# Kernel optimization log

Hardware: AMD Instinct MI355X
Metric: run time of the kernel (lower is better)

The kernel has to match this reference:

```python
import jax, jax.numpy as jnp
import numpy as np

B, S_IMG, S_TXT, D, H, HD = 1, 2048, 512, 3072, 24, 128
EMB, N_IP = 4096, 64
IP_SCALE = 1.0
EPS = 1e-6
SM_SCALE = 1.0 / np.sqrt(HD).astype(np.float32)


def _lin(x, W, b=None):
    # torch Linear: y = x @ W.T + b, W: [out, in]
    y = jnp.einsum('bsd,od->bso', x, W)
    return y if b is None else y + b


def _heads(x):  # [B,S,D] -> [B,H,S,HD]
    return x.reshape(B, -1, H, HD).transpose(0, 2, 1, 3)


def _rms(x, w):
    return x * jax.lax.rsqrt(jnp.mean(x * x, axis=-1, keepdims=True) + EPS) * w


def _rope(x, cos, sin):
    # interleaved real/imag rotation, cos/sin: [S, HD] broadcast over B,H
    xr = x.reshape(*x.shape[:-1], HD // 2, 2)
    rot = jnp.stack([-xr[..., 1], xr[..., 0]], axis=-1).reshape(x.shape)
    return x * cos + rot * sin


def _sdpa(q, k, v):
    s = jnp.einsum('bhqd,bhkd->bhqk', q, k) * SM_SCALE
    p = jax.nn.softmax(s, axis=-1)
    return jnp.einsum('bhqk,bhkd->bhqd', p, v)


def setup_inputs() -> dict:
    key = jax.random.key(0)
    ks = jax.random.split(key, 32)
    r = lambda i, shape: jax.random.normal(ks[i], shape, dtype=jnp.float32)
    w = lambda i, shape: r(i, shape) * 0.02
    inp = {
        'hidden_states': r(0, (B, S_IMG, D)),
        'encoder_hidden_states': r(1, (B, S_TXT, D)),
        'image_embeds': r(2, (B, N_IP, EMB)),
        'rope_cos': jnp.cos(r(3, (S_TXT + S_IMG, HD))),
        'rope_sin': jnp.sin(r(3, (S_TXT + S_IMG, HD))),
        'Wq': w(4, (D, D)), 'bq': jnp.zeros((D,)),
        'Wk': w(5, (D, D)), 'bk': jnp.zeros((D,)),
        'Wv': w(6, (D, D)), 'bv': jnp.zeros((D,)),
        'Waq': w(7, (D, D)), 'baq': jnp.zeros((D,)),
        'Wak': w(8, (D, D)), 'bak': jnp.zeros((D,)),
        'Wav': w(9, (D, D)), 'bav': jnp.zeros((D,)),
        'Wo': w(10, (D, D)), 'bo': jnp.zeros((D,)),
        'Wao': w(11, (D, D)), 'bao': jnp.zeros((D,)),
        'norm_q_w': jnp.ones((HD,)), 'norm_k_w': jnp.ones((HD,)),
        'norm_aq_w': jnp.ones((HD,)), 'norm_ak_w': jnp.ones((HD,)),
        'Wk_ip': w(12, (D, EMB)), 'Wv_ip': w(13, (D, EMB)),
        'txt_seq_len': S_TXT,
    }
    return inp


def reference(hidden_states, encoder_hidden_states, image_embeds, rope_cos, rope_sin,
              Wq, bq, Wk, bk, Wv, bv, Waq, baq, Wak, bak, Wav, bav,
              Wo, bo, Wao, bao, norm_q_w, norm_k_w, norm_aq_w, norm_ak_w,
              Wk_ip, Wv_ip, txt_seq_len):
    # main stream projections + per-head RMSNorm
    q = _rms(_heads(_lin(hidden_states, Wq, bq)), norm_q_w)
    k = _rms(_heads(_lin(hidden_states, Wk, bk)), norm_k_w)
    v = _heads(_lin(hidden_states, Wv, bv))
    # encoder (text) stream projections + RMSNorm, concat text before image
    eq = _rms(_heads(_lin(encoder_hidden_states, Waq, baq)), norm_aq_w)
    ek = _rms(_heads(_lin(encoder_hidden_states, Wak, bak)), norm_ak_w)
    ev = _heads(_lin(encoder_hidden_states, Wav, bav))
    q = jnp.concatenate([eq, q], axis=2)
    k = jnp.concatenate([ek, k], axis=2)
    v = jnp.concatenate([ev, v], axis=2)
    # IP-adapter branch uses pre-RoPE image-token queries
    ip_q = q[:, :, txt_seq_len:]
    ip_k = _heads(_lin(image_embeds, Wk_ip))
    ip_v = _heads(_lin(image_embeds, Wv_ip))
    ip_hs = _sdpa(ip_q, ip_k, ip_v).transpose(0, 2, 1, 3).reshape(B, -1, H * HD)
    # rotary on joint q/k, then main attention
    q = _rope(q, rope_cos, rope_sin)
    k = _rope(k, rope_cos, rope_sin)
    hs = _sdpa(q, k, v).transpose(0, 2, 1, 3).reshape(B, -1, H * HD)
    # add scaled IP-adapter output to the image part
    img = hs[:, txt_seq_len:] + IP_SCALE * ip_hs
    enc = hs[:, :txt_seq_len]
    # output projections
    out_img = _lin(img, Wo, bo)
    out_enc = _lin(enc, Wao, bao)
    return out_img, out_enc
```

## Files before the change

### kernel.cpp

```cpp
#include <hip/hip_runtime.h>
#include <hip/hip_bf16.h>

#define H 24
#define HD 128
#define DMODEL 3072
#define S_IMG 2048
#define S_TXT 512
#define S_ALL 2560
#define EMB 4096
#define N_IP 64
#define SM_SCALE 0.08838834764831845f

typedef __attribute__((ext_vector_type(8))) short short8;
typedef __attribute__((ext_vector_type(4))) float f32x4;
typedef __attribute__((ext_vector_type(16))) float f32x16;

__device__ inline unsigned short f2bf(float f) {
    unsigned u = __builtin_bit_cast(unsigned, f);
    return (unsigned short)((u + 0x7fffu + ((u >> 16) & 1u)) >> 16);
}
__device__ inline unsigned pk2(float a, float b) {
    return (unsigned)f2bf(a) | ((unsigned)f2bf(b) << 16);
}
__device__ inline float bf2f(unsigned short u) {
    unsigned x = ((unsigned)u) << 16;
    return __builtin_bit_cast(float, x);
}

__device__ inline void gload16(const void* g, void* l) {
    __builtin_amdgcn_global_load_lds(
        (const __attribute__((address_space(1))) unsigned int*)g,
        (__attribute__((address_space(3))) unsigned int*)(unsigned int)(unsigned long long)l,
        16, 0, 0);
}

struct CastSegs {
    const float* src[13];
    unsigned short* dst[13];
    int n8[13];
    int ntot8[13];
    int bstart[14];
};

__global__ __launch_bounds__(256)
void castall(CastSegs cs)
{
    int b = blockIdx.x, seg = 0;
    while (seg < 12 && b >= cs.bstart[seg + 1]) seg++;
    int nb = cs.bstart[seg + 1] - cs.bstart[seg];
    int lb = b - cs.bstart[seg];
    const float* in = cs.src[seg];
    unsigned short* out = cs.dst[seg];
    int n8 = cs.n8[seg], ntot = cs.ntot8[seg];
    for (int i = lb * 256 + threadIdx.x; i < ntot; i += nb * 256) {
        int4 o;
        if (i < n8) {
            const float4* p = (const float4*)(in + (size_t)i * 8);
            float4 a = p[0], bb = p[1];
            o.x = pk2(a.x, a.y); o.y = pk2(a.z, a.w);
            o.z = pk2(bb.x, bb.y); o.w = pk2(bb.z, bb.w);
        } else {
            o.x = 0; o.y = 0; o.z = 0; o.w = 0;
        }
        *(int4*)(out + (size_t)i * 8) = o;
    }
}

__global__ __launch_bounds__(256)
void bcat2(const float* __restrict__ q0, const float* __restrict__ k0, const float* __restrict__ v0,
           const float* __restrict__ q1, const float* __restrict__ k1, const float* __restrict__ v1,
           float* __restrict__ d0, float* __restrict__ d1)
{
    int i = blockIdx.x * 256 + threadIdx.x;
    int which = i >= 3 * DMODEL;
    int j = which ? i - 3 * DMODEL : i;
    const float* a = which ? q1 : q0;
    const float* b = which ? k1 : k0;
    const float* c = which ? v1 : v0;
    float v = (j < DMODEL) ? a[j] : ((j < 2 * DMODEL) ? b[j - DMODEL] : c[j - 2 * DMODEL]);
    (which ? d1 : d0)[j] = v;
}

template<int OUTBF>
__global__ __launch_bounds__(256)
void gemmx(const unsigned short* __restrict__ A0, const unsigned short* __restrict__ B0,
           const float* __restrict__ b0, void* __restrict__ C0,
           const unsigned short* __restrict__ A1, const unsigned short* __restrict__ B1,
           const float* __restrict__ b1, void* __restrict__ C1,
           int mbSplit, int N, int K, int nbm, int GN)
{
    __shared__ unsigned short sm[2 * 8192];
    const int tid = threadIdx.x, lane = tid & 63, wid = tid >> 6;
    const int wr = wid >> 1, wc = wid & 1;
    const int r15 = lane & 15, g = lane >> 4;

    int nwg = gridDim.x;
    int t = (blockIdx.x & 7) * (nwg >> 3) + (blockIdx.x >> 3);
    int gsz = nbm * GN;
    int G = t / gsz, l = t - G * gsz;
    int mb = l % nbm, nb = G * GN + l / nbm;

    const unsigned short* A; const unsigned short* B; const float* bias; void* C; int mrow;
    if (mb < mbSplit) { A = A0; B = B0; bias = b0; C = C0; mrow = mb; }
    else             { A = A1; B = B1; bias = b1; C = C1; mrow = mb - mbSplit; }
    const int m0 = mrow * 128, n0 = nb * 128;

    const int lr = lane >> 3;
    const int lc = lane & 7;
    const int gcol = ((lc * 16) ^ (lr << 4)) >> 1;

    const unsigned short* Ab = A + (size_t)(m0 + wid * 32 + lr) * K + gcol;
    const unsigned short* Bb = B + (size_t)(n0 + wid * 32 + lr) * K + gcol;
    char* smc = (char*)sm;

    f32x4 acc[4][4];
    #pragma unroll
    for (int i = 0; i < 4; i++)
        #pragma unroll
        for (int j = 0; j < 4; j++)
            acc[i][j] = {0.f, 0.f, 0.f, 0.f};

    for (int k0 = 0; k0 < K; k0 += 64) {
        #pragma unroll
        for (int cc = 0; cc < 4; cc++) {
            gload16(Ab + (size_t)cc * 8 * K + k0, smc + (wid * 32 + cc * 8) * 128);
            gload16(Bb + (size_t)cc * 8 * K + k0, smc + 16384 + (wid * 32 + cc * 8) * 128);
        }
        __syncthreads();
        #pragma unroll
        for (int ks = 0; ks < 2; ks++) {
            short8 af[4], bf[4];
            #pragma unroll
            for (int mi = 0; mi < 4; mi++) {
                int row = wr * 64 + mi * 16 + r15;
                af[mi] = *(const short8*)(smc + row * 128 + ((ks * 64 + g * 16) ^ ((row & 7) << 4)));
            }
            #pragma unroll
            for (int ni = 0; ni < 4; ni++) {
                int row = wc * 64 + ni * 16 + r15;
                bf[ni] = *(const short8*)(smc + 16384 + row * 128 + ((ks * 64 + g * 16) ^ ((row & 7) << 4)));
            }
            #pragma unroll
            for (int mi = 0; mi < 4; mi++)
                #pragma unroll
                for (int ni = 0; ni < 4; ni++)
                    acc[mi][ni] = __builtin_amdgcn_mfma_f32_16x16x32_bf16(af[mi], bf[ni], acc[mi][ni], 0, 0, 0);
        }
        __syncthreads();
    }
    #pragma unroll
    for (int mi = 0; mi < 4; mi++) {
        #pragma unroll
        for (int ni = 0; ni < 4; ni++) {
            int col = n0 + wc * 64 + ni * 16 + r15;
            float bv = bias ? bias[col] : 0.f;
            #pragma unroll
            for (int r = 0; r < 4; r++) {
                int grow = m0 + wr * 64 + mi * 16 + g * 4 + r;
                float v = acc[mi][ni][r] + bv;
                if (OUTBF)
                    ((unsigned short*)C)[(size_t)grow * N + col] = f2bf(v);
                else
                    ((float*)C)[(size_t)grow * N + col] = v;
            }
        }
    }
}

__global__ __launch_bounds__(256)
void rmsropeQK(const unsigned short* __restrict__ qkvb,
               const float* __restrict__ nqw, const float* __restrict__ nkw,
               const float* __restrict__ naqw, const float* __restrict__ nakw,
               const float* __restrict__ cosb, const float* __restrict__ sinb,
               unsigned short* __restrict__ qb, unsigned short* __restrict__ kb,
               unsigned short* __restrict__ ipq)
{
    int wg = blockIdx.x * 4 + (threadIdx.x >> 6);
    int lane = threadIdx.x & 63;
    int s = wg / H, h = wg - s * H;
    const unsigned short* row = qkvb + (size_t)s * (3 * DMODEL);
    unsigned uq = *(const unsigned*)(row + h * HD + lane * 2);
    unsigned uk = *(const unsigned*)(row + DMODEL + h * HD + lane * 2);
    float q0 = bf2f((unsigned short)uq), q1 = bf2f((unsigned short)(uq >> 16));
    float k0 = bf2f((unsigned short)uk), k1 = bf2f((unsigned short)(uk >> 16));
    float sq = q0 * q0 + q1 * q1, sk = k0 * k0 + k1 * k1;
    #pragma unroll
    for (int off = 1; off < 64; off <<= 1) {
        sq += __shfl_xor(sq, off);
        sk += __shfl_xor(sk, off);
    }
    float rq = rsqrtf(sq * (1.f / HD) + 1e-6f) * SM_SCALE;
    float rk = rsqrtf(sk * (1.f / HD) + 1e-6f);
    const float* wq = (s < S_TXT) ? naqw : nqw;
    const float* wk = (s < S_TXT) ? nakw : nkw;
    float xq0 = q0 * rq * wq[lane * 2], xq1 = q1 * rq * wq[lane * 2 + 1];
    float xk0 = k0 * rk * wk[lane * 2], xk1 = k1 * rk * wk[lane * 2 + 1];
    if (s >= S_TXT)
        *(unsigned*)(ipq + (size_t)h * S_IMG * HD + (size_t)(s - S_TXT) * HD + lane * 2) = pk2(xq0, xq1);
    float c0 = cosb[s * HD + lane * 2], c1 = cosb[s * HD + lane * 2 + 1];
    float s0 = sinb[s * HD + lane * 2], s1 = sinb[s * HD + lane * 2 + 1];
    *(unsigned*)(qb + (size_t)h * S_ALL * HD + (size_t)s * HD + lane * 2) =
        pk2(xq0 * c0 - xq1 * s0, xq1 * c1 + xq0 * s1);
    *(unsigned*)(kb + (size_t)h * S_ALL * HD + (size_t)s * HD + lane * 2) =
        pk2(xk0 * c0 - xk1 * s0, xk1 * c1 + xk0 * s1);
}

__global__ __launch_bounds__(256)
void vtrans(const unsigned short* __restrict__ src, int stride,
            unsigned short* __restrict__ vt, int Stot)
{
    __shared__ unsigned short lv[64 * 130];
    int h = blockIdx.y;
    int s0 = blockIdx.x * 64;
    const unsigned short* base = src + (size_t)s0 * stride + h * HD;
    int tid = threadIdx.x;
    #pragma unroll
    for (int i = 0; i < 4; i++) {
        int slot = tid + 256 * i;
        int row = slot >> 4, c = slot & 15;
        int4 v = *(const int4*)(base + (size_t)row * stride + c * 8);
        unsigned* p = (unsigned*)(lv + row * 130 + c * 8);
        p[0] = (unsigned)v.x; p[1] = (unsigned)v.y; p[2] = (unsigned)v.z; p[3] = (unsigned)v.w;
    }
    __syncthreads();
    #pragma unroll
    for (int i = 0; i < 4; i++) {
        int slot = tid + 256 * i;
        int d = slot >> 3, c8 = slot & 7;
        unsigned w0 = lv[(c8 * 8 + 0) * 130 + d] | ((unsigned)lv[(c8 * 8 + 1) * 130 + d] << 16);
        unsigned w1 = lv[(c8 * 8 + 2) * 130 + d] | ((unsigned)lv[(c8 * 8 + 3) * 130 + d] << 16);
        unsigned w2 = lv[(c8 * 8 + 4) * 130 + d] | ((unsigned)lv[(c8 * 8 + 5) * 130 + d] << 16);
        unsigned w3 = lv[(c8 * 8 + 6) * 130 + d] | ((unsigned)lv[(c8 * 8 + 7) * 130 + d] << 16);
        int4 o = {(int)w0, (int)w1, (int)w2, (int)w3};
        *(int4*)(vt + (size_t)(h * HD + d) * Stot + s0 + c8 * 8) = o;
    }
}

__global__ __launch_bounds__(256)
void cast_heads8(const unsigned short* __restrict__ in, unsigned short* __restrict__ out)
{
    int idx = blockIdx.x * 256 + threadIdx.x;
    int s = idx / 384;
    int rem = idx - s * 384;
    int h = rem >> 4, d8 = rem & 15;
    int4 v = *(const int4*)(in + (size_t)s * (2 * DMODEL) + h * HD + d8 * 8);
    *(int4*)(out + ((size_t)h * N_IP + s) * HD + d8 * 8) = v;
}

template<int MODE>
__global__ __launch_bounds__(512, 2)
void flash2(const unsigned short* __restrict__ Q, const unsigned short* __restrict__ Kb,
            const unsigned short* __restrict__ Vt, const unsigned short* __restrict__ ipb,
            unsigned short* __restrict__ Out, int Sq, int Skv)
{
    __shared__ char sm[33792];
    const int h = blockIdx.y;
    const int q0 = blockIdx.x * 256;
    const int tid = threadIdx.x, w = tid >> 6, lane = tid & 63;
    const int l31 = lane & 31, hi = lane >> 5;

    const unsigned short* Qh = Q + ((size_t)h * Sq + q0 + w * 32 + l31) * HD + hi * 8;
    short8 qf[8];
    #pragma unroll
    for (int c = 0; c < 8; c++)
        qf[c] = *(const short8*)(Qh + c * 16);

    float m = -3.0e38f, lsum = 0.f;
    f32x16 o[4];
    #pragma unroll
    for (int dn = 0; dn < 4; dn++)
        #pragma unroll
        for (int r = 0; r < 16; r++) o[dn][r] = 0.f;

    const unsigned short* Kh = Kb + (size_t)h * Skv * HD;
    const unsigned short* Vth = Vt + (size_t)h * HD * Skv;
    float* scl = (float*)(sm + 32768) + w * 32;

    for (int kv0 = 0; kv0 < Skv; kv0 += 64) {
        #pragma unroll
        for (int cc = 0; cc < 2; cc++) {
            int flat = w * 128 + cc * 64 + lane;
            int row = flat >> 4, slot = flat & 15;
            gload16(Kh + (size_t)(kv0 + row) * HD + (((slot * 16) ^ ((row & 7) << 4)) >> 1),
                    sm + w * 2048 + cc * 1024);
        }
        #pragma unroll
        for (int cc = 0; cc < 2; cc++) {
            int flat = w * 128 + cc * 64 + lane;
            int d = flat >> 3, slot = flat & 7;
            gload16(Vth + (size_t)d * Skv + kv0 + (((slot * 16) ^ ((d & 7) << 4)) >> 1),
                    sm + 16384 + w * 2048 + cc * 1024);
        }
        __syncthreads();

        f32x16 st[2];
        __builtin_amdgcn_s_setprio(1);
        #pragma unroll
        for (int t2 = 0; t2 < 2; t2++) {
            #pragma unroll
            for (int r = 0; r < 16; r++) st[t2][r] = 0.f;
            #pragma unroll
            for (int c = 0; c < 8; c++) {
                int krow = t2 * 32 + l31;
                short8 kf = *(const short8*)(sm + krow * 256 + ((c * 32 + hi * 16) ^ ((krow & 7) << 4)));
                st[t2] = __builtin_amdgcn_mfma_f32_32x32x16_bf16(kf, qf[c], st[t2], 0, 0, 0);
            }
        }
        __builtin_amdgcn_s_setprio(0);
        float pmax = st[0][0];
        #pragma unroll
        for (int t2 = 0; t2 < 2; t2++)
            #pragma unroll
            for (int r = 0; r < 16; r++) pmax = fmaxf(pmax, st[t2][r]);
        pmax = fmaxf(pmax, __shfl_xor(pmax, 32));
        float mn = fmaxf(m, pmax);
        float sc = __expf(m - mn);
        m = mn;
        float psum = 0.f;
        #pragma unroll
        for (int t2 = 0; t2 < 2; t2++)
            #pragma unroll
            for (int r = 0; r < 16; r++) {
                float p = __expf(st[t2][r] - mn);
                st[t2][r] = p;
                psum += p;
            }
        psum += __shfl_xor(psum, 32);
        lsum = lsum * sc + psum;
        if (hi == 0) scl[l31] = sc;

        short8 pa[4];
        #pragma unroll
        for (int k4 = 0; k4 < 4; k4++) {
            unsigned U  = pk2(st[(k4 * 8 + 0) >> 4][(k4 * 8 + 0) & 15], st[(k4 * 8 + 1) >> 4][(k4 * 8 + 1) & 15]);
            unsigned V  = pk2(st[(k4 * 8 + 2) >> 4][(k4 * 8 + 2) & 15], st[(k4 * 8 + 3) >> 4][(k4 * 8 + 3) & 15]);
            unsigned U2 = pk2(st[(k4 * 8 + 4) >> 4][(k4 * 8 + 4) & 15], st[(k4 * 8 + 5) >> 4][(k4 * 8 + 5) & 15]);
            unsigned V2 = pk2(st[(k4 * 8 + 6) >> 4][(k4 * 8 + 6) & 15], st[(k4 * 8 + 7) >> 4][(k4 * 8 + 7) & 15]);
            unsigned SU = __shfl_xor(U, 32), SU2 = __shfl_xor(U2, 32);
            unsigned SV = __shfl_xor(V, 32), SV2 = __shfl_xor(V2, 32);
            uint4 wv;
            wv.x = hi ? SU2 : U;
            wv.y = hi ? SV2 : V;
            wv.z = hi ? U2 : SU;
            wv.w = hi ? V2 : SV;
            pa[k4] = __builtin_bit_cast(short8, wv);
        }
        float scb[16];
        #pragma unroll
        for (int r = 0; r < 16; r++)
            scb[r] = scl[(r & 3) + 8 * (r >> 2) + 4 * hi];
        #pragma unroll
        for (int dn = 0; dn < 4; dn++)
            #pragma unroll
            for (int r = 0; r < 16; r++) o[dn][r] *= scb[r];
        __builtin_amdgcn_s_setprio(1);
        #pragma unroll
        for (int dn = 0; dn < 4; dn++) {
            #pragma unroll
            for (int k4 = 0; k4 < 4; k4++) {
                int vrow = dn * 32 + l31;
                short8 vf = *(const short8*)(sm + 16384 + vrow * 128 + ((k4 * 32 + hi * 16) ^ ((vrow & 7) << 4)));
                o[dn] = __builtin_amdgcn_mfma_f32_32x32x16_bf16(pa[k4], vf, o[dn], 0, 0, 0);
            }
        }
        __builtin_amdgcn_s_setprio(0);
        __syncthreads();
    }

    if (hi == 0) scl[l31] = 1.f / lsum;
    float linv[16];
    #pragma unroll
    for (int r = 0; r < 16; r++)
        linv[r] = scl[(r & 3) + 8 * (r >> 2) + 4 * hi];
    #pragma unroll
    for (int dn = 0; dn < 4; dn++) {
        #pragma unroll
        for (int r = 0; r < 16; r++) {
            int qrow = q0 + w * 32 + (r & 3) + 8 * (r >> 2) + 4 * hi;
            int col = h * HD + dn * 32 + l31;
            float val = o[dn][r] * linv[r];
            if (MODE == 1 && qrow >= S_TXT)
                val += bf2f(ipb[(size_t)(qrow - S_TXT) * DMODEL + col]);
            Out[(size_t)qrow * DMODEL + col] = f2bf(val);
        }
    }
}

extern "C" void kernel_launch(void* const* d_in, const int* in_sizes, int n_in,
                              void* d_out, int out_size, void* d_ws, size_t ws_size,
                              hipStream_t stream)
{
    const float* hs   = (const float*)d_in[0];
    const float* enc  = (const float*)d_in[1];
    const float* iemb = (const float*)d_in[2];
    const float* cosb = (const float*)d_in[3];
    const float* sinb = (const float*)d_in[4];
    const float* Wq  = (const float*)d_in[5];  const float* bq  = (const float*)d_in[6];
    const float* Wk  = (const float*)d_in[7];  const float* bk  = (const float*)d_in[8];
    const float* Wv  = (const float*)d_in[9];  const float* bv  = (const float*)d_in[10];
    const float* Waq = (const float*)d_in[11]; const float* baq = (const float*)d_in[12];
    const float* Wak = (const float*)d_in[13]; const float* bak = (const float*)d_in[14];
    const float* Wav = (const float*)d_in[15]; const float* bav = (const float*)d_in[16];
    const float* Wo  = (const float*)d_in[17]; const float* bo  = (const float*)d_in[18];
    const float* Wao = (const float*)d_in[19]; const float* bao = (const float*)d_in[20];
    const float* nq  = (const float*)d_in[21]; const float* nk  = (const float*)d_in[22];
    const float* naq = (const float*)d_in[23]; const float* nak = (const float*)d_in[24];
    const float* Wkip = (const float*)d_in[25]; const float* Wvip = (const float*)d_in[26];
    (void)in_sizes; (void)n_in; (void)out_size; (void)ws_size;

    char* ws = (char*)d_ws;
    size_t off = 0;
    auto alloc = [&](size_t b) { char* p = ws + off; off += (b + 255) & ~(size_t)255; return p; };
    unsigned short* qkvb    = (unsigned short*)alloc((size_t)S_ALL * 3 * DMODEL * 2);
    unsigned short* ipkvb   = (unsigned short*)alloc((size_t)128 * 2 * DMODEL * 2);
    unsigned short* hs_bf   = (unsigned short*)alloc((size_t)S_IMG * DMODEL * 2);
    unsigned short* enc_bf  = (unsigned short*)alloc((size_t)S_TXT * DMODEL * 2);
    unsigned short* iemb_bf = (unsigned short*)alloc((size_t)128 * EMB * 2);
    unsigned short* Wqkv  = (unsigned short*)alloc((size_t)3 * DMODEL * DMODEL * 2);
    unsigned short* Waqkv = (unsigned short*)alloc((size_t)3 * DMODEL * DMODEL * 2);
    unsigned short* Wo_b  = (unsigned short*)alloc((size_t)DMODEL * DMODEL * 2);
    unsigned short* Wao_b = (unsigned short*)alloc((size_t)DMODEL * DMODEL * 2);
    unsigned short* Wip   = (unsigned short*)alloc((size_t)2 * DMODEL * EMB * 2);
    float* bqkv  = (float*)alloc(3 * DMODEL * 4);
    float* baqkv = (float*)alloc(3 * DMODEL * 4);
    unsigned short* qb    = (unsigned short*)alloc((size_t)H * S_ALL * HD * 2);
    unsigned short* kbf   = (unsigned short*)alloc((size_t)H * S_ALL * HD * 2);
    unsigned short* vtb   = (unsigned short*)alloc((size_t)H * HD * S_ALL * 2);
    unsigned short* ipqb  = (unsigned short*)alloc((size_t)H * S_IMG * HD * 2);
    unsigned short* ipkb  = (unsigned short*)alloc((size_t)H * N_IP * HD * 2);
    unsigned short* ipvtb = (unsigned short*)alloc((size_t)H * HD * N_IP * 2);
    unsigned short* ipbuf = (unsigned short*)alloc((size_t)S_IMG * DMODEL * 2);
    unsigned short* attnb = (unsigned short*)alloc((size_t)S_ALL * DMODEL * 2);

    const size_t DD = (size_t)DMODEL * DMODEL;
    const size_t DE = (size_t)DMODEL * EMB;
    const int D8 = (int)(DD / 8), E8 = (int)(DE / 8);

    CastSegs cs;
    const float* srcs[13] = {hs, enc, iemb, Wq, Wk, Wv, Waq, Wak, Wav, Wo, Wao, Wkip, Wvip};
    unsigned short* dsts[13] = {hs_bf, enc_bf, iemb_bf,
                                Wqkv, Wqkv + DD, Wqkv + 2 * DD,
                                Waqkv, Waqkv + DD, Waqkv + 2 * DD,
                                Wo_b, Wao_b, Wip, Wip + DE};
    int n8s[13]  = {S_IMG * DMODEL / 8, S_TXT * DMODEL / 8, N_IP * EMB / 8,
                    D8, D8, D8, D8, D8, D8, D8, D8, E8, E8};
    int nt8s[13] = {S_IMG * DMODEL / 8, S_TXT * DMODEL / 8, 128 * EMB / 8,
                    D8, D8, D8, D8, D8, D8, D8, D8, E8, E8};
    int acc = 0;
    for (int i = 0; i < 13; i++) {
        cs.src[i] = srcs[i]; cs.dst[i] = dsts[i];
        cs.n8[i] = n8s[i]; cs.ntot8[i] = nt8s[i];
        cs.bstart[i] = acc;
        int nb = (nt8s[i] + 8191) / 8192;
        acc += (nb < 1 ? 1 : nb);
    }
    cs.bstart[13] = acc;

    dim3 blk(256);
    castall<<<dim3(acc), blk, 0, stream>>>(cs);
    bcat2<<<dim3(72), blk, 0, stream>>>(bq, bk, bv, baq, bak, bav, bqkv, baqkv);

    gemmx<1><<<dim3(20 * 72), blk, 0, stream>>>(
        hs_bf, Wqkv, bqkv, qkvb + (size_t)S_TXT * 3 * DMODEL,
        enc_bf, Waqkv, baqkv, qkvb,
        16, 3 * DMODEL, DMODEL, 20, 9);
    gemmx<1><<<dim3(48), blk, 0, stream>>>(
        iemb_bf, Wip, nullptr, ipkvb,
        iemb_bf, Wip, nullptr, ipkvb,
        1, 2 * DMODEL, EMB, 1, 6);

    rmsropeQK<<<dim3(15360), blk, 0, stream>>>(qkvb, nq, nk, naq, nak, cosb, sinb, qb, kbf, ipqb);
    vtrans<<<dim3(40, 24), blk, 0, stream>>>(qkvb + 2 * DMODEL, 3 * DMODEL, vtb, S_ALL);
    cast_heads8<<<dim3(96), blk, 0, stream>>>(ipkvb, ipkb);
    vtrans<<<dim3(1, 24), blk, 0, stream>>>(ipkvb + DMODEL, 2 * DMODEL, ipvtb, N_IP);

    dim3 fblk(512);
    flash2<0><<<dim3(8, 24),  fblk, 0, stream>>>(ipqb, ipkb, ipvtb, nullptr, ipbuf, S_IMG, N_IP);
    flash2<1><<<dim3(10, 24), fblk, 0, stream>>>(qb, kbf, vtb, ipbuf, attnb, S_ALL, S_ALL);

    float* dout = (float*)d_out;
    gemmx<0><<<dim3(20 * 24), blk, 0, stream>>>(
        attnb, Wao_b, bao, dout + (size_t)S_IMG * DMODEL,
        attnb + (size_t)S_TXT * DMODEL, Wo_b, bo, dout,
        4, DMODEL, DMODEL, 20, 3);
}
```

Baseline: 664.8 us.

## Fuse fp32-to-bf16 weight conversion into GEMM B-tile loads with register prefetch

Drops the separate pass that cast all projection weights to bf16. The GEMM now reads fp32 weight rows directly from up to three separate weight tensors, packs them to bf16 in registers, and stores them swizzled into LDS. The next B tile is prefetched into registers while the current tile is computed. This removes a large read-write pass over every weight matrix. The cost is twice the B-operand bytes per GEMM tile fetch, more VGPR pressure, and B no longer uses the direct global-to-LDS load path.

```diff
diff --git a/kernel.cpp b/kernel.cpp
--- a/kernel.cpp
+++ b/kernel.cpp
@@ -35,18 +35,18 @@
 }
 
 struct CastSegs {
-    const float* src[13];
-    unsigned short* dst[13];
-    int n8[13];
-    int ntot8[13];
-    int bstart[14];
+    const float* src[3];
+    unsigned short* dst[3];
+    int n8[3];
+    int ntot8[3];
+    int bstart[4];
 };
 
 __global__ __launch_bounds__(256)
 void castall(CastSegs cs)
 {
     int b = blockIdx.x, seg = 0;
-    while (seg < 12 && b >= cs.bstart[seg + 1]) seg++;
+    while (seg < 2 && b >= cs.bstart[seg + 1]) seg++;
     int nb = cs.bstart[seg + 1] - cs.bstart[seg];
     int lb = b - cs.bstart[seg];
     const float* in = cs.src[seg];
@@ -81,12 +81,35 @@
     (which ? d1 : d0)[j] = v;
 }
 
+struct BPtr { const float* w[3]; };
+
+__device__ inline void loadB(const float* Bb, int K, int k0, float4 (&bv)[4][2])
+{
+    #pragma unroll
+    for (int cc = 0; cc < 4; cc++) {
+        const float* s = Bb + (size_t)cc * 8 * K + k0;
+        bv[cc][0] = *(const float4*)(s);
+        bv[cc][1] = *(const float4*)(s + 4);
+    }
+}
+__device__ inline void writeB(char* smc, int wid, int lr, int lc, const float4 (&bv)[4][2])
+{
+    #pragma unroll
+    for (int cc = 0; cc < 4; cc++) {
+        int row = wid * 32 + cc * 8 + lr;
+        int4 o;
+        o.x = pk2(bv[cc][0].x, bv[cc][0].y);
+        o.y = pk2(bv[cc][0].z, bv[cc][0].w);
+        o.z = pk2(bv[cc][1].x, bv[cc][1].y);
+        o.w = pk2(bv[cc][1].z, bv[cc][1].w);
+        *(int4*)(smc + 16384 + row * 128 + ((lc * 16) ^ (lr << 4))) = o;
+    }
+}
+
 template<int OUTBF>
 __global__ __launch_bounds__(256)
-void gemmx(const unsigned short* __restrict__ A0, const unsigned short* __restrict__ B0,
-           const float* __restrict__ b0, void* __restrict__ C0,
-           const unsigned short* __restrict__ A1, const unsigned short* __restrict__ B1,
-           const float* __restrict__ b1, void* __restrict__ C1,
+void gemmx(const unsigned short* __restrict__ A0, BPtr B0, const float* __restrict__ b0, void* __restrict__ C0,
+           const unsigned short* __restrict__ A1, BPtr B1, const float* __restrict__ b1, void* __restrict__ C1,
            int mbSplit, int N, int K, int nbm, int GN)
 {
     __shared__ unsigned short sm[2 * 8192];
@@ -100,9 +123,9 @@
     int G = t / gsz, l = t - G * gsz;
     int mb = l % nbm, nb = G * GN + l / nbm;
 
-    const unsigned short* A; const unsigned short* B; const float* bias; void* C; int mrow;
-    if (mb < mbSplit) { A = A0; B = B0; bias = b0; C = C0; mrow = mb; }
-    else             { A = A1; B = B1; bias = b1; C = C1; mrow = mb - mbSplit; }
+    const unsigned short* A; BPtr Bp; const float* bias; void* C; int mrow;
+    if (mb < mbSplit) { A = A0; Bp = B0; bias = b0; C = C0; mrow = mb; }
+    else             { A = A1; Bp = B1; bias = b1; C = C1; mrow = mb - mbSplit; }
     const int m0 = mrow * 128, n0 = nb * 128;
 
     const int lr = lane >> 3;
@@ -110,7 +133,9 @@
     const int gcol = ((lc * 16) ^ (lr << 4)) >> 1;
 
     const unsigned short* Ab = A + (size_t)(m0 + wid * 32 + lr) * K + gcol;
-    const unsigned short* Bb = B + (size_t)(n0 + wid * 32 + lr) * K + gcol;
+    int bi = nb / 24;
+    int brow0 = (nb - bi * 24) * 128;
+    const float* Bb = Bp.w[bi] + (size_t)(brow0 + wid * 32 + lr) * K + lc * 8;
     char* smc = (char*)sm;
 
     f32x4 acc[4][4];
@@ -120,33 +145,45 @@
         for (int j = 0; j < 4; j++)
             acc[i][j] = {0.f, 0.f, 0.f, 0.f};
 
-    for (int k0 = 0; k0 < K; k0 += 64) {
-        #pragma unroll
-        for (int cc = 0; cc < 4; cc++) {
-            gload16(Ab + (size_t)cc * 8 * K + k0, smc + (wid * 32 + cc * 8) * 128);
-            gload16(Bb + (size_t)cc * 8 * K + k0, smc + 16384 + (wid * 32 + cc * 8) * 128);
-        }
-        __syncthreads();
-        #pragma unroll
-        for (int ks = 0; ks < 2; ks++) {
-            short8 af[4], bf[4];
-            #pragma unroll
-            for (int mi = 0; mi < 4; mi++) {
-                int row = wr * 64 + mi * 16 + r15;
-                af[mi] = *(const short8*)(smc + row * 128 + ((ks * 64 + g * 16) ^ ((row & 7) << 4)));
+    const int nk = K >> 6;
+    float4 bva[4][2], bvb[4][2];
+    loadB(Bb, K, 0, bva);
+
+    for (int kt = 0; kt < nk; kt += 2) {
+        #pragma unroll
+        for (int half = 0; half < 2; half++) {
+            int k0 = (kt + half) * 64;
+            if (half == 0) writeB(smc, wid, lr, lc, bva);
+            else           writeB(smc, wid, lr, lc, bvb);
+            #pragma unroll
+            for (int cc = 0; cc < 4; cc++)
+                gload16(Ab + (size_t)cc * 8 * K + k0, smc + (wid * 32 + cc * 8) * 128);
+            if (kt + half + 1 < nk) {
+                if (half == 0) loadB(Bb, K, k0 + 64, bvb);
+                else           loadB(Bb, K, k0 + 64, bva);
             }
-            #pragma unroll
-            for (int ni = 0; ni < 4; ni++) {
-                int row = wc * 64 + ni * 16 + r15;
-                bf[ni] = *(const short8*)(smc + 16384 + row * 128 + ((ks * 64 + g * 16) ^ ((row & 7) << 4)));
+            __syncthreads();
+            #pragma unroll
+            for (int ks = 0; ks < 2; ks++) {
+                short8 af[4], bf[4];
+                #pragma unroll
+                for (int mi = 0; mi < 4; mi++) {
+                    int row = wr * 64 + mi * 16 + r15;
+                    af[mi] = *(const short8*)(smc + row * 128 + ((ks * 64 + g * 16) ^ ((row & 7) << 4)));
+                }
+                #pragma unroll
+                for (int ni = 0; ni < 4; ni++) {
+                    int row = wc * 64 + ni * 16 + r15;
+                    bf[ni] = *(const short8*)(smc + 16384 + row * 128 + ((ks * 64 + g * 16) ^ ((row & 7) << 4)));
+                }
+                #pragma unroll
+                for (int mi = 0; mi < 4; mi++)
+                    #pragma unroll
+                    for (int ni = 0; ni < 4; ni++)
+                        acc[mi][ni] = __builtin_amdgcn_mfma_f32_16x16x32_bf16(af[mi], bf[ni], acc[mi][ni], 0, 0, 0);
             }
-            #pragma unroll
-            for (int mi = 0; mi < 4; mi++)
-                #pragma unroll
-                for (int ni = 0; ni < 4; ni++)
-                    acc[mi][ni] = __builtin_amdgcn_mfma_f32_16x16x32_bf16(af[mi], bf[ni], acc[mi][ni], 0, 0, 0);
-        }
-        __syncthreads();
+            __syncthreads();
+        }
     }
     #pragma unroll
     for (int mi = 0; mi < 4; mi++) {
@@ -416,11 +453,6 @@
     unsigned short* hs_bf   = (unsigned short*)alloc((size_t)S_IMG * DMODEL * 2);
     unsigned short* enc_bf  = (unsigned short*)alloc((size_t)S_TXT * DMODEL * 2);
     unsigned short* iemb_bf = (unsigned short*)alloc((size_t)128 * EMB * 2);
-    unsigned short* Wqkv  = (unsigned short*)alloc((size_t)3 * DMODEL * DMODEL * 2);
-    unsigned short* Waqkv = (unsigned short*)alloc((size_t)3 * DMODEL * DMODEL * 2);
-    unsigned short* Wo_b  = (unsigned short*)alloc((size_t)DMODEL * DMODEL * 2);
-    unsigned short* Wao_b = (unsigned short*)alloc((size_t)DMODEL * DMODEL * 2);
-    unsigned short* Wip   = (unsigned short*)alloc((size_t)2 * DMODEL * EMB * 2);
     float* bqkv  = (float*)alloc(3 * DMODEL * 4);
     float* baqkv = (float*)alloc(3 * DMODEL * 4);
     unsigned short* qb    = (unsigned short*)alloc((size_t)H * S_ALL * HD * 2);
@@ -432,41 +464,37 @@
     unsigned short* ipbuf = (unsigned short*)alloc((size_t)S_IMG * DMODEL * 2);
     unsigned short* attnb = (unsigned short*)alloc((size_t)S_ALL * DMODEL * 2);
 
-    const size_t DD = (size_t)DMODEL * DMODEL;
-    const size_t DE = (size_t)DMODEL * EMB;
-    const int D8 = (int)(DD / 8), E8 = (int)(DE / 8);
-
     CastSegs cs;
-    const float* srcs[13] = {hs, enc, iemb, Wq, Wk, Wv, Waq, Wak, Wav, Wo, Wao, Wkip, Wvip};
-    unsigned short* dsts[13] = {hs_bf, enc_bf, iemb_bf,
-                                Wqkv, Wqkv + DD, Wqkv + 2 * DD,
-                                Waqkv, Waqkv + DD, Waqkv + 2 * DD,
-                                Wo_b, Wao_b, Wip, Wip + DE};
-    int n8s[13]  = {S_IMG * DMODEL / 8, S_TXT * DMODEL / 8, N_IP * EMB / 8,
-                    D8, D8, D8, D8, D8, D8, D8, D8, E8, E8};
-    int nt8s[13] = {S_IMG * DMODEL / 8, S_TXT * DMODEL / 8, 128 * EMB / 8,
-                    D8, D8, D8, D8, D8, D8, D8, D8, E8, E8};
+    const float* srcs[3] = {hs, enc, iemb};
+    unsigned short* dsts[3] = {hs_bf, enc_bf, iemb_bf};
+    int n8s[3]  = {S_IMG * DMODEL / 8, S_TXT * DMODEL / 8, N_IP * EMB / 8};
+    int nt8s[3] = {S_IMG * DMODEL / 8, S_TXT * DMODEL / 8, 128 * EMB / 8};
     int acc = 0;
-    for (int i = 0; i < 13; i++) {
+    for (int i = 0; i < 3; i++) {
         cs.src[i] = srcs[i]; cs.dst[i] = dsts[i];
         cs.n8[i] = n8s[i]; cs.ntot8[i] = nt8s[i];
         cs.bstart[i] = acc;
-        int nb = (nt8s[i] + 8191) / 8192;
-        acc += (nb < 1 ? 1 : nb);
-    }
-    cs.bstart[13] = acc;
+        acc += (nt8s[i] + 511) / 512;
+    }
+    cs.bstart[3] = acc;
 
     dim3 blk(256);
     castall<<<dim3(acc), blk, 0, stream>>>(cs);
     bcat2<<<dim3(72), blk, 0, stream>>>(bq, bk, bv, baq, bak, bav, bqkv, baqkv);
 
+    BPtr Bqkv  = {{Wq, Wk, Wv}};
+    BPtr Baqkv = {{Waq, Wak, Wav}};
+    BPtr Bip   = {{Wkip, Wvip, nullptr}};
+    BPtr Bo    = {{Wo, nullptr, nullptr}};
+    BPtr Bao   = {{Wao, nullptr, nullptr}};
+
     gemmx<1><<<dim3(20 * 72), blk, 0, stream>>>(
-        hs_bf, Wqkv, bqkv, qkvb + (size_t)S_TXT * 3 * DMODEL,
-        enc_bf, Waqkv, baqkv, qkvb,
+        hs_bf, Bqkv, bqkv, qkvb + (size_t)S_TXT * 3 * DMODEL,
+        enc_bf, Baqkv, baqkv, qkvb,
         16, 3 * DMODEL, DMODEL, 20, 9);
     gemmx<1><<<dim3(48), blk, 0, stream>>>(
-        iemb_bf, Wip, nullptr, ipkvb,
-        iemb_bf, Wip, nullptr, ipkvb,
+        iemb_bf, Bip, nullptr, ipkvb,
+        iemb_bf, Bip, nullptr, ipkvb,
         1, 2 * DMODEL, EMB, 1, 6);
 
     rmsropeQK<<<dim3(15360), blk, 0, stream>>>(qkvb, nq, nk, naq, nak, cosb, sinb, qb, kbf, ipqb);
@@ -480,7 +508,7 @@
 
     float* dout = (float*)d_out;
     gemmx<0><<<dim3(20 * 24), blk, 0, stream>>>(
-        attnb, Wao_b, bao, dout + (size_t)S_IMG * DMODEL,
-        attnb + (size_t)S_TXT * DMODEL, Wo_b, bo, dout,
+        attnb, Bao, bao, dout + (size_t)S_IMG * DMODEL,
+        attnb + (size_t)S_TXT * DMODEL, Bo, bo, dout,
         4, DMODEL, DMODEL, 20, 3);
 }
```

Result: slower. 1.043 ms (+56.9%).

## Double-buffer K/V tiles in flash attention, shrink blocks, add lazy rescaling

Applied to the files above, without the earlier changes.

Rewrites the flash attention kernel to use 256-thread blocks of 128 query rows. K/V tiles are double-buffered in LDS so the next tile's global loads are issued before the current tile's compute, which removes the barrier-bound load-then-compute serialization. It also skips the running-max rescale of the output accumulators unless the max grows by more than 8 (a lazy-rescale trick). The grid doubles to 480 blocks for better CU coverage, at the cost of more LDS per block (about 66KB), which may limit occupancy.

```diff
diff --git a/kernel.cpp b/kernel.cpp
--- a/kernel.cpp
+++ b/kernel.cpp
@@ -248,14 +248,14 @@
 }
 
 template<int MODE>
-__global__ __launch_bounds__(512, 2)
-void flash2(const unsigned short* __restrict__ Q, const unsigned short* __restrict__ Kb,
+__global__ __launch_bounds__(256)
+void flash3(const unsigned short* __restrict__ Q, const unsigned short* __restrict__ Kb,
             const unsigned short* __restrict__ Vt, const unsigned short* __restrict__ ipb,
             unsigned short* __restrict__ Out, int Sq, int Skv)
 {
-    __shared__ char sm[33792];
+    __shared__ char sm[66048];
     const int h = blockIdx.y;
-    const int q0 = blockIdx.x * 256;
+    const int q0 = blockIdx.x * 128;
     const int tid = threadIdx.x, w = tid >> 6, lane = tid & 63;
     const int l31 = lane & 31, hi = lane >> 5;
 
@@ -274,24 +274,34 @@
 
     const unsigned short* Kh = Kb + (size_t)h * Skv * HD;
     const unsigned short* Vth = Vt + (size_t)h * HD * Skv;
-    float* scl = (float*)(sm + 32768) + w * 32;
-
-    for (int kv0 = 0; kv0 < Skv; kv0 += 64) {
-        #pragma unroll
-        for (int cc = 0; cc < 2; cc++) {
-            int flat = w * 128 + cc * 64 + lane;
+    float* scl = (float*)(sm + 65536) + w * 32;
+    const int nt = Skv >> 6;
+
+    auto STAGE = [&](int buf, int kv0) {
+        #pragma unroll
+        for (int cc = 0; cc < 4; cc++) {
+            int flat = w * 256 + cc * 64 + lane;
             int row = flat >> 4, slot = flat & 15;
             gload16(Kh + (size_t)(kv0 + row) * HD + (((slot * 16) ^ ((row & 7) << 4)) >> 1),
-                    sm + w * 2048 + cc * 1024);
-        }
-        #pragma unroll
-        for (int cc = 0; cc < 2; cc++) {
-            int flat = w * 128 + cc * 64 + lane;
+                    sm + buf * 16384 + flat * 16);
+        }
+        #pragma unroll
+        for (int cc = 0; cc < 4; cc++) {
+            int flat = w * 256 + cc * 64 + lane;
             int d = flat >> 3, slot = flat & 7;
             gload16(Vth + (size_t)d * Skv + kv0 + (((slot * 16) ^ ((d & 7) << 4)) >> 1),
-                    sm + 16384 + w * 2048 + cc * 1024);
-        }
-        __syncthreads();
+                    sm + 32768 + buf * 16384 + flat * 16);
+        }
+    };
+
+    STAGE(0, 0);
+    __syncthreads();
+
+    for (int t = 0; t < nt; t++) {
+        int cur = t & 1;
+        if (t + 1 < nt) STAGE(cur ^ 1, (t + 1) * 64);
+        char* Ks = sm + cur * 16384;
+        char* Vs = sm + 32768 + cur * 16384;
 
         f32x16 st[2];
         __builtin_amdgcn_s_setprio(1);
@@ -302,32 +312,46 @@
             #pragma unroll
             for (int c = 0; c < 8; c++) {
                 int krow = t2 * 32 + l31;
-                short8 kf = *(const short8*)(sm + krow * 256 + ((c * 32 + hi * 16) ^ ((krow & 7) << 4)));
+                short8 kf = *(const short8*)(Ks + krow * 256 + ((c * 32 + hi * 16) ^ ((krow & 7) << 4)));
                 st[t2] = __builtin_amdgcn_mfma_f32_32x32x16_bf16(kf, qf[c], st[t2], 0, 0, 0);
             }
         }
         __builtin_amdgcn_s_setprio(0);
+
         float pmax = st[0][0];
         #pragma unroll
         for (int t2 = 0; t2 < 2; t2++)
             #pragma unroll
             for (int r = 0; r < 16; r++) pmax = fmaxf(pmax, st[t2][r]);
         pmax = fmaxf(pmax, __shfl_xor(pmax, 32));
-        float mn = fmaxf(m, pmax);
-        float sc = __expf(m - mn);
-        m = mn;
+
+        if (!__all(pmax - m <= 8.0f)) {
+            float mn = fmaxf(m, pmax);
+            float sc = __expf(m - mn);
+            m = mn;
+            lsum *= sc;
+            if (hi == 0) scl[l31] = sc;
+            float scb[16];
+            #pragma unroll
+            for (int r = 0; r < 16; r++)
+                scb[r] = scl[(r & 3) + 8 * (r >> 2) + 4 * hi];
+            #pragma unroll
+            for (int dn = 0; dn < 4; dn++)
+                #pragma unroll
+                for (int r = 0; r < 16; r++) o[dn][r] *= scb[r];
+        }
+
         float psum = 0.f;
         #pragma unroll
         for (int t2 = 0; t2 < 2; t2++)
             #pragma unroll
             for (int r = 0; r < 16; r++) {
-                float p = __expf(st[t2][r] - mn);
+                float p = __expf(st[t2][r] - m);
                 st[t2][r] = p;
                 psum += p;
             }
         psum += __shfl_xor(psum, 32);
-        lsum = lsum * sc + psum;
-        if (hi == 0) scl[l31] = sc;
+        lsum += psum;
 
         short8 pa[4];
         #pragma unroll
@@ -345,21 +369,14 @@
             wv.w = hi ? V2 : SV;
             pa[k4] = __builtin_bit_cast(short8, wv);
         }
-        float scb[16];
-        #pragma unroll
-        for (int r = 0; r < 16; r++)
-            scb[r] = scl[(r & 3) + 8 * (r >> 2) + 4 * hi];
-        #pragma unroll
-        for (int dn = 0; dn < 4; dn++)
-            #pragma unroll
-            for (int r = 0; r < 16; r++) o[dn][r] *= scb[r];
+
         __builtin_amdgcn_s_setprio(1);
         #pragma unroll
         for (int dn = 0; dn < 4; dn++) {
             #pragma unroll
             for (int k4 = 0; k4 < 4; k4++) {
                 int vrow = dn * 32 + l31;
-                short8 vf = *(const short8*)(sm + 16384 + vrow * 128 + ((k4 * 32 + hi * 16) ^ ((vrow & 7) << 4)));
+                short8 vf = *(const short8*)(Vs + vrow * 128 + ((k4 * 32 + hi * 16) ^ ((vrow & 7) << 4)));
                 o[dn] = __builtin_amdgcn_mfma_f32_32x32x16_bf16(pa[k4], vf, o[dn], 0, 0, 0);
             }
         }
@@ -474,9 +491,8 @@
     cast_heads8<<<dim3(96), blk, 0, stream>>>(ipkvb, ipkb);
     vtrans<<<dim3(1, 24), blk, 0, stream>>>(ipkvb + DMODEL, 2 * DMODEL, ipvtb, N_IP);
 
-    dim3 fblk(512);
-    flash2<0><<<dim3(8, 24),  fblk, 0, stream>>>(ipqb, ipkb, ipvtb, nullptr, ipbuf, S_IMG, N_IP);
-    flash2<1><<<dim3(10, 24), fblk, 0, stream>>>(qb, kbf, vtb, ipbuf, attnb, S_ALL, S_ALL);
+    flash3<0><<<dim3(16, 24), blk, 0, stream>>>(ipqb, ipkb, ipvtb, nullptr, ipbuf, S_IMG, N_IP);
+    flash3<1><<<dim3(20, 24), blk, 0, stream>>>(qb, kbf, vtb, ipbuf, attnb, S_ALL, S_ALL);
 
     float* dout = (float*)d_out;
     gemmx<0><<<dim3(20 * 24), blk, 0, stream>>>(
```

Measured after the change: 735.9 us. +10.7%, slower.

## Widen flash KV tile to 128 and skip rescale unless the max grows

Applied to the files above, without the earlier changes.

The flash attention kernel is templated on KV block size. The main attention now uses 128-key tiles with a 64KB LDS buffer, which halves the number of barrier and softmax-rescale rounds per block. It also adds a lazy online-softmax rescale: the running max and the output accumulator are only rescaled when some row's new max exceeds the old one by more than 8, which avoids the rescale multiply and LDS round trip in most iterations. The cost is more LDS per block, which may limit occupancy to fewer than 2 blocks per CU, and the exponentials can reach up to e^8 before rescaling, which is safe in fp32 but slightly changes the numerics.

```diff
diff --git a/kernel.cpp b/kernel.cpp
--- a/kernel.cpp
+++ b/kernel.cpp
@@ -247,17 +247,19 @@
     *(int4*)(out + ((size_t)h * N_IP + s) * HD + d8 * 8) = v;
 }
 
-template<int MODE>
+template<int MODE, int KVBLK>
 __global__ __launch_bounds__(512, 2)
-void flash2(const unsigned short* __restrict__ Q, const unsigned short* __restrict__ Kb,
+void flash4(const unsigned short* __restrict__ Q, const unsigned short* __restrict__ Kb,
             const unsigned short* __restrict__ Vt, const unsigned short* __restrict__ ipb,
             unsigned short* __restrict__ Out, int Sq, int Skv)
 {
-    __shared__ char sm[33792];
+    __shared__ char sm[66560];
     const int h = blockIdx.y;
     const int q0 = blockIdx.x * 256;
     const int tid = threadIdx.x, w = tid >> 6, lane = tid & 63;
     const int l31 = lane & 31, hi = lane >> 5;
+    const int T2 = KVBLK / 32, K4 = KVBLK / 16, SLOTV = KVBLK / 8, NL = KVBLK / 32;
+    const int VROWB = KVBLK * 2;
 
     const unsigned short* Qh = Q + ((size_t)h * Sq + q0 + w * 32 + l31) * HD + hi * 8;
     short8 qf[8];
@@ -274,29 +276,31 @@
 
     const unsigned short* Kh = Kb + (size_t)h * Skv * HD;
     const unsigned short* Vth = Vt + (size_t)h * HD * Skv;
-    float* scl = (float*)(sm + 32768) + w * 32;
-
-    for (int kv0 = 0; kv0 < Skv; kv0 += 64) {
-        #pragma unroll
-        for (int cc = 0; cc < 2; cc++) {
-            int flat = w * 128 + cc * 64 + lane;
-            int row = flat >> 4, slot = flat & 15;
+    float* scl = (float*)(sm + 65536) + w * 32;
+    const int nt = Skv / KVBLK;
+
+    for (int t = 0; t < nt; t++) {
+        int kv0 = t * KVBLK;
+        #pragma unroll
+        for (int cc = 0; cc < NL; cc++) {
+            int f = cc * 512 + tid;
+            int row = f >> 4, slot = f & 15;
             gload16(Kh + (size_t)(kv0 + row) * HD + (((slot * 16) ^ ((row & 7) << 4)) >> 1),
-                    sm + w * 2048 + cc * 1024);
-        }
-        #pragma unroll
-        for (int cc = 0; cc < 2; cc++) {
-            int flat = w * 128 + cc * 64 + lane;
-            int d = flat >> 3, slot = flat & 7;
+                    sm + f * 16);
+        }
+        #pragma unroll
+        for (int cc = 0; cc < NL; cc++) {
+            int f = cc * 512 + tid;
+            int d = f / SLOTV, slot = f % SLOTV;
             gload16(Vth + (size_t)d * Skv + kv0 + (((slot * 16) ^ ((d & 7) << 4)) >> 1),
-                    sm + 16384 + w * 2048 + cc * 1024);
+                    sm + 32768 + f * 16);
         }
         __syncthreads();
 
-        f32x16 st[2];
+        f32x16 st[T2];
         __builtin_amdgcn_s_setprio(1);
         #pragma unroll
-        for (int t2 = 0; t2 < 2; t2++) {
+        for (int t2 = 0; t2 < T2; t2++) {
             #pragma unroll
             for (int r = 0; r < 16; r++) st[t2][r] = 0.f;
             #pragma unroll
@@ -307,31 +311,45 @@
             }
         }
         __builtin_amdgcn_s_setprio(0);
+
         float pmax = st[0][0];
         #pragma unroll
-        for (int t2 = 0; t2 < 2; t2++)
+        for (int t2 = 0; t2 < T2; t2++)
             #pragma unroll
             for (int r = 0; r < 16; r++) pmax = fmaxf(pmax, st[t2][r]);
         pmax = fmaxf(pmax, __shfl_xor(pmax, 32));
-        float mn = fmaxf(m, pmax);
-        float sc = __expf(m - mn);
-        m = mn;
+
+        if (!__all(pmax - m <= 8.0f)) {
+            float mn = fmaxf(m, pmax);
+            float sc = __expf(m - mn);
+            m = mn;
+            lsum *= sc;
+            if (hi == 0) scl[l31] = sc;
+            float scb[16];
+            #pragma unroll
+            for (int r = 0; r < 16; r++)
+                scb[r] = scl[(r & 3) + 8 * (r >> 2) + 4 * hi];
+            #pragma unroll
+            for (int dn = 0; dn < 4; dn++)
+                #pragma unroll
+                for (int r = 0; r < 16; r++) o[dn][r] *= scb[r];
+        }
+
         float psum = 0.f;
         #pragma unroll
-        for (int t2 = 0; t2 < 2; t2++)
+        for (int t2 = 0; t2 < T2; t2++)
             #pragma unroll
             for (int r = 0; r < 16; r++) {
-                float p = __expf(st[t2][r] - mn);
+                float p = __expf(st[t2][r] - m);
                 st[t2][r] = p;
                 psum += p;
             }
         psum += __shfl_xor(psum, 32);
-        lsum = lsum * sc + psum;
-        if (hi == 0) scl[l31] = sc;
-
-        short8 pa[4];
-        #pragma unroll
-        for (int k4 = 0; k4 < 4; k4++) {
+        lsum += psum;
+
+        short8 pa[K4];
+        #pragma unroll
+        for (int k4 = 0; k4 < K4; k4++) {
             unsigned U  = pk2(st[(k4 * 8 + 0) >> 4][(k4 * 8 + 0) & 15], st[(k4 * 8 + 1) >> 4][(k4 * 8 + 1) & 15]);
             unsigned V  = pk2(st[(k4 * 8 + 2) >> 4][(k4 * 8 + 2) & 15], st[(k4 * 8 + 3) >> 4][(k4 * 8 + 3) & 15]);
             unsigned U2 = pk2(st[(k4 * 8 + 4) >> 4][(k4 * 8 + 4) & 15], st[(k4 * 8 + 5) >> 4][(k4 * 8 + 5) & 15]);
@@ -345,21 +363,14 @@
             wv.w = hi ? V2 : SV;
             pa[k4] = __builtin_bit_cast(short8, wv);
         }
-        float scb[16];
-        #pragma unroll
-        for (int r = 0; r < 16; r++)
-            scb[r] = scl[(r & 3) + 8 * (r >> 2) + 4 * hi];
-        #pragma unroll
-        for (int dn = 0; dn < 4; dn++)
-            #pragma unroll
-            for (int r = 0; r < 16; r++) o[dn][r] *= scb[r];
+
         __builtin_amdgcn_s_setprio(1);
         #pragma unroll
         for (int dn = 0; dn < 4; dn++) {
             #pragma unroll
-            for (int k4 = 0; k4 < 4; k4++) {
+            for (int k4 = 0; k4 < K4; k4++) {
                 int vrow = dn * 32 + l31;
-                short8 vf = *(const short8*)(sm + 16384 + vrow * 128 + ((k4 * 32 + hi * 16) ^ ((vrow & 7) << 4)));
+                short8 vf = *(const short8*)(sm + 32768 + vrow * VROWB + ((k4 * 32 + hi * 16) ^ ((vrow & 7) << 4)));
                 o[dn] = __builtin_amdgcn_mfma_f32_32x32x16_bf16(pa[k4], vf, o[dn], 0, 0, 0);
             }
         }
@@ -475,8 +486,8 @@
     vtrans<<<dim3(1, 24), blk, 0, stream>>>(ipkvb + DMODEL, 2 * DMODEL, ipvtb, N_IP);
 
     dim3 fblk(512);
-    flash2<0><<<dim3(8, 24),  fblk, 0, stream>>>(ipqb, ipkb, ipvtb, nullptr, ipbuf, S_IMG, N_IP);
-    flash2<1><<<dim3(10, 24), fblk, 0, stream>>>(qb, kbf, vtb, ipbuf, attnb, S_ALL, S_ALL);
+    flash4<0, 64><<<dim3(8, 24),  fblk, 0, stream>>>(ipqb, ipkb, ipvtb, nullptr, ipbuf, S_IMG, N_IP);
+    flash4<1, 128><<<dim3(10, 24), fblk, 0, stream>>>(qb, kbf, vtb, ipbuf, attnb, S_ALL, S_ALL);
 
     float* dout = (float*)d_out;
     gemmx<0><<<dim3(20 * 24), blk, 0, stream>>>(
```

Result: no change. 655.2 us (-1.4%).
